# Optimization experiments

Hardware: AMD Instinct MI355X
Metric: run time of the kernel (lower is better)

The kernel has to match this reference:

```python
import jax, jax.numpy as jnp
import numpy as np

B, T, C = 4, 2048, 1024
H, D = 16, 64  # num_heads, head_dim
SCALE = D ** -0.5


def setup_inputs() -> dict:
    key = jax.random.key(0)
    ks = jax.random.split(key, 6)
    s = 0.02
    return {
        "hidden_states": jax.random.normal(ks[0], (B, T, C), dtype=jnp.float32),
        "wq": jax.random.normal(ks[1], (C, C), dtype=jnp.float32) * s,
        "wk": jax.random.normal(ks[2], (C, C), dtype=jnp.float32) * s,
        "wv": jax.random.normal(ks[3], (C, C), dtype=jnp.float32) * s,
        "wo": jax.random.normal(ks[4], (C, C), dtype=jnp.float32) * s,
        "bo": jnp.zeros((C,), dtype=jnp.float32),
    }


def reference(hidden_states, wq, wk, wv, wo, bo):
    b, t, c = hidden_states.shape
    # torch nn.Linear: y = x @ W^T
    q = hidden_states @ wq.T
    k = hidden_states @ wk.T
    v = hidden_states @ wv.T
    # (b, t, c) -> (b, h, t, d)
    q = q.reshape(b, t, H, D).transpose(0, 2, 1, 3)
    k = k.reshape(b, t, H, D).transpose(0, 2, 1, 3)
    v = v.reshape(b, t, H, D).transpose(0, 2, 1, 3)
    scores = jnp.einsum("bhqd,bhkd->bhqk", q, k) * SCALE
    attn = jax.nn.softmax(scores, axis=-1)
    out = jnp.einsum("bhqk,bhkd->bhqd", attn, v)
    out = out.transpose(0, 2, 1, 3).reshape(b, t, c)
    return out @ wo.T + bo
```

## Files before the change

### kernel.cpp

```cpp
#include <hip/hip_runtime.h>
#include <hip/hip_bf16.h>
#include <stdint.h>
#include <math.h>

#define Bb 4
#define Tt 2048
#define Cc 1024
#define Hh 16
#define Dd 64
#define Mm (Bb * Tt)
#define KVB 64
#define NT (Tt / KVB)

typedef __attribute__((ext_vector_type(8))) short bf8;
typedef __attribute__((ext_vector_type(4))) float f32x4;
typedef __attribute__((ext_vector_type(16))) float f32x16;
typedef __attribute__((ext_vector_type(8))) float f32x8v;
typedef __attribute__((ext_vector_type(2))) float f32x2v;
typedef __attribute__((ext_vector_type(8))) unsigned short u16x8;

#define QSCALE 0.1803368801111244f
#define M_FIX 4.0f

__device__ __forceinline__ unsigned short f2bf(float f) {
  __hip_bfloat16 h = __float2bfloat16(f);
  return *reinterpret_cast<unsigned short*>(&h);
}
__device__ __forceinline__ float bf2f(unsigned short s) {
  union { unsigned u; float f; } v; v.u = ((unsigned)s) << 16;
  return v.f;
}
__device__ __forceinline__ float fexp2(float x) {
#if __has_builtin(__builtin_amdgcn_exp2f)
  return __builtin_amdgcn_exp2f(x);
#else
  return exp2f(x);
#endif
}
__device__ __forceinline__ unsigned cvtpk(float lo, float hi) {
  unsigned r;
  asm volatile("v_cvt_pk_bf16_f32 %0, %1, %2" : "=v"(r) : "v"(lo), "v"(hi));
  return r;
}
__device__ __forceinline__ void gl_lds16(const void* g, void* l) {
  __builtin_amdgcn_global_load_lds(
      (const __attribute__((address_space(1))) void*)g,
      (__attribute__((address_space(3))) void*)l, 16, 0, 0);
}

__global__ __launch_bounds__(256) void cast_all(
    const float* __restrict__ hs, const float* __restrict__ wq,
    const float* __restrict__ wk, const float* __restrict__ wv,
    const float* __restrict__ wo, unsigned short* __restrict__ Xb,
    unsigned short* __restrict__ Wbase) {
  long long g = (long long)(blockIdx.x * 256 + threadIdx.x) * 8;
  const float* src;
  unsigned short* dst;
  long long off;
  const long long HS = 8LL * 1024 * 1024;
  if (g < HS) {
    src = hs; dst = Xb; off = g;
  } else {
    long long r = g - HS;
    int wsel = (int)(r >> 20);
    off = r & ((1LL << 20) - 1);
    src = (wsel == 0) ? wq : (wsel == 1) ? wk : (wsel == 2) ? wv : wo;
    dst = Wbase + ((long long)wsel << 20);
  }
  const float4* p = (const float4*)(src + off);
  float4 a = p[0], b = p[1];
  u16x8 o;
  o[0] = f2bf(a.x); o[1] = f2bf(a.y); o[2] = f2bf(a.z); o[3] = f2bf(a.w);
  o[4] = f2bf(b.x); o[5] = f2bf(b.y); o[6] = f2bf(b.z); o[7] = f2bf(b.w);
  *(u16x8*)(dst + off) = o;
}

template <int MODE>
__global__ __launch_bounds__(256, 2)
void gemm_bt(const unsigned short* __restrict__ A,
             const unsigned short* __restrict__ Bw,
             void* __restrict__ Cout,
             const float* __restrict__ bias,
             int M, int N, int K) {
  __shared__ unsigned short As[128 * 32];
  __shared__ unsigned short Bs[128 * 32];
  const int tid = threadIdx.x;
  const int lane = tid & 63;
  const int w = tid >> 6;
  const int wr = w >> 1, wc = w & 1;
  const int row0 = blockIdx.y * 128;
  const int col0 = blockIdx.x * 128;
  const int lr = lane & 15;
  const int lk = (lane >> 4) * 8;

  f32x4 acc[4][4] = {};

  const int sr = tid >> 2;
  const int sc = (tid & 3) * 8;

  for (int k0 = 0; k0 < K; k0 += 32) {
    gl_lds16(A  + (size_t)(row0 + sr) * K + k0 + sc,      &As[sr * 32 + sc]);
    gl_lds16(A  + (size_t)(row0 + 64 + sr) * K + k0 + sc, &As[(64 + sr) * 32 + sc]);
    gl_lds16(Bw + (size_t)(col0 + sr) * K + k0 + sc,      &Bs[sr * 32 + sc]);
    gl_lds16(Bw + (size_t)(col0 + 64 + sr) * K + k0 + sc, &Bs[(64 + sr) * 32 + sc]);
    __syncthreads();

    bf8 a[4], b[4];
#pragma unroll
    for (int mi = 0; mi < 4; ++mi)
      a[mi] = *(const bf8*)&As[(wr * 64 + mi * 16 + lr) * 32 + lk];
#pragma unroll
    for (int ni = 0; ni < 4; ++ni)
      b[ni] = *(const bf8*)&Bs[(wc * 64 + ni * 16 + lr) * 32 + lk];
#pragma unroll
    for (int mi = 0; mi < 4; ++mi)
#pragma unroll
      for (int ni = 0; ni < 4; ++ni)
        acc[mi][ni] = __builtin_amdgcn_mfma_f32_16x16x32_bf16(
            a[mi], b[ni], acc[mi][ni], 0, 0, 0);
    __syncthreads();
  }

#pragma unroll
  for (int mi = 0; mi < 4; ++mi) {
#pragma unroll
    for (int ni = 0; ni < 4; ++ni) {
      const int col = col0 + wc * 64 + ni * 16 + lr;
      const int rowb = row0 + wr * 64 + mi * 16 + (lane >> 4) * 4;
      if (MODE == 1) {
#pragma unroll
        for (int r = 0; r < 4; ++r)
          ((float*)Cout)[(size_t)(rowb + r) * N + col] = acc[mi][ni][r] + bias[col];
      } else {
        unsigned short* outb = (unsigned short*)Cout;
        if (col < 2048) {
          unsigned short* dst = outb + (col < 1024 ? 0 : 8 * 1024 * 1024);
          const int c = col & 1023;
#pragma unroll
          for (int r = 0; r < 4; ++r)
            dst[(size_t)(rowb + r) * 1024 + c] = f2bf(acc[mi][ni][r]);
        } else {
          const int c = col - 2048;
          const int bidx = rowb >> 11, t0 = rowb & 2047;
          const int hh = c >> 6, dd = c & 63;
          uint2 pk;
          pk.x = (unsigned)f2bf(acc[mi][ni][0]) | ((unsigned)f2bf(acc[mi][ni][1]) << 16);
          pk.y = (unsigned)f2bf(acc[mi][ni][2]) | ((unsigned)f2bf(acc[mi][ni][3]) << 16);
          size_t addr = (((size_t)(bidx * Hh + hh)) * Dd + dd) * (size_t)Tt + t0;
          *(uint2*)(outb + 16 * 1024 * 1024 + addr) = pk;
        }
      }
    }
  }
}

__global__ __launch_bounds__(512, 2)
void flash_attn(const unsigned short* __restrict__ Q,
                const unsigned short* __restrict__ Km,
                const unsigned short* __restrict__ Vt,
                unsigned short* __restrict__ O) {
  __shared__ unsigned short smem[3 * 8192];

  const int tid = threadIdx.x;
  const int lane = tid & 63;
  const int w = tid >> 6;
  const int bh = blockIdx.x;
  const int qt = blockIdx.y;
  const int b = bh >> 4, h = bh & 15;
  const size_t base = (size_t)b * Tt * Cc + (size_t)h * Dd;
  const size_t vtbase = (size_t)bh * Dd * Tt;
  const int r31 = lane & 31, hi = lane >> 5;
  const int qrow = qt * 256 + w * 32 + r31;
  const int sw = r31 & 7;

  int coh[4];
#pragma unroll
  for (int ks = 0; ks < 4; ++ks) coh[ks] = ((2 * ks + hi) ^ sw) * 8;

  bf8 qb[4];
#pragma unroll
  for (int ks = 0; ks < 4; ++ks) {
    bf8 t = *(const bf8*)(Q + base + (size_t)qrow * Cc + ks * 16 + hi * 8);
#pragma unroll
    for (int i = 0; i < 8; ++i)
      qb[ks][i] = (short)f2bf(bf2f((unsigned short)t[i]) * QSCALE);
  }

  float l_r = 0.f;
  f32x16 o_acc[2];
#pragma unroll
  for (int dt = 0; dt < 2; ++dt) o_acc[dt] = (f32x16)0.0f;

  const int strow = tid >> 3;
  const int stch = tid & 7;
  const unsigned short* ksrc = Km + base + (size_t)strow * Cc + ((stch ^ (strow & 7)) * 8);
  const unsigned short* vsrc = Vt + vtbase + (size_t)strow * Tt + ((stch ^ (strow & 7)) * 8);

  gl_lds16(ksrc,                   &smem[0 * 8192 + tid * 8]);
  gl_lds16(vsrc,                   &smem[0 * 8192 + 4096 + tid * 8]);
  gl_lds16(ksrc + (size_t)KVB * Cc, &smem[1 * 8192 + tid * 8]);
  gl_lds16(vsrc + KVB,             &smem[1 * 8192 + 4096 + tid * 8]);
  asm volatile("s_waitcnt vmcnt(2)" ::: "memory");
  __builtin_amdgcn_sched_barrier(0);
  __builtin_amdgcn_s_barrier();
  __builtin_amdgcn_sched_barrier(0);

  int cur = 0;
  for (int t = 0; t < NT; ++t) {
    if (t + 2 < NT) {
      int nb = cur + 2; if (nb >= 3) nb -= 3;
      const int kb = (t + 2) * KVB;
      gl_lds16(ksrc + (size_t)kb * Cc, &smem[nb * 8192 + tid * 8]);
      gl_lds16(vsrc + kb,              &smem[nb * 8192 + 4096 + tid * 8]);
    }

    const unsigned short* ksl = &smem[cur * 8192];
    const unsigned short* vsl = &smem[cur * 8192 + 4096];

    f32x16 s0 = (f32x16)0.0f, s1 = (f32x16)0.0f;
    __builtin_amdgcn_s_setprio(1);
#pragma unroll
    for (int ks = 0; ks < 4; ++ks) {
      bf8 kf = *(const bf8*)&ksl[r31 * 64 + coh[ks]];
      s0 = __builtin_amdgcn_mfma_f32_32x32x16_bf16(kf, qb[ks], s0, 0, 0, 0);
    }
#pragma unroll
    for (int ks = 0; ks < 4; ++ks) {
      bf8 kf = *(const bf8*)&ksl[(32 + r31) * 64 + coh[ks]];
      s1 = __builtin_amdgcn_mfma_f32_32x32x16_bf16(kf, qb[ks], s1, 0, 0, 0);
    }
    __builtin_amdgcn_s_setprio(0);

    s0 = s0 - M_FIX;
    s1 = s1 - M_FIX;
#pragma unroll
    for (int j = 0; j < 16; ++j) { s0[j] = fexp2(s0[j]); s1[j] = fexp2(s1[j]); }
    {
      f32x16 t16 = s0 + s1;
      f32x8v t8v = __builtin_shufflevector(t16, t16, 0, 1, 2, 3, 4, 5, 6, 7) +
                   __builtin_shufflevector(t16, t16, 8, 9, 10, 11, 12, 13, 14, 15);
      f32x4 t4v = __builtin_shufflevector(t8v, t8v, 0, 1, 2, 3) +
                  __builtin_shufflevector(t8v, t8v, 4, 5, 6, 7);
      f32x2v t2v = __builtin_shufflevector(t4v, t4v, 0, 1) +
                   __builtin_shufflevector(t4v, t4v, 2, 3);
      float ps = t2v[0] + t2v[1];
      ps += __shfl_xor(ps, 32);
      l_r += ps;
    }

    unsigned U[8][2];
#pragma unroll
    for (int k = 0; k < 4; ++k) {
      U[k][0] = cvtpk(s0[4 * k],     s0[4 * k + 1]);
      U[k][1] = cvtpk(s0[4 * k + 2], s0[4 * k + 3]);
      U[4 + k][0] = cvtpk(s1[4 * k],     s1[4 * k + 1]);
      U[4 + k][1] = cvtpk(s1[4 * k + 2], s1[4 * k + 3]);
    }
    bf8 pb[4];
#pragma unroll
    for (int ks = 0; ks < 4; ++ks) {
      unsigned a0 = U[2 * ks][0], b0 = U[2 * ks + 1][0];
      asm volatile("v_permlane32_swap_b32 %0, %1" : "+v"(a0), "+v"(b0));
      unsigned a1 = U[2 * ks][1], b1 = U[2 * ks + 1][1];
      asm volatile("v_permlane32_swap_b32 %0, %1" : "+v"(a1), "+v"(b1));
      union { unsigned u[4]; bf8 v; } pk_;
      pk_.u[0] = a0; pk_.u[1] = a1; pk_.u[2] = b0; pk_.u[3] = b1;
      pb[ks] = pk_.v;
    }

    __builtin_amdgcn_s_setprio(1);
#pragma unroll
    for (int dt = 0; dt < 2; ++dt) {
      f32x16 z = o_acc[dt];
#pragma unroll
      for (int ks = 0; ks < 4; ++ks) {
        bf8 vf = *(const bf8*)&vsl[(dt * 32 + r31) * 64 + coh[ks]];
        z = __builtin_amdgcn_mfma_f32_32x32x16_bf16(vf, pb[ks], z, 0, 0, 0);
      }
      o_acc[dt] = z;
    }
    __builtin_amdgcn_s_setprio(0);

    if (t + 2 < NT) {
      asm volatile("s_waitcnt vmcnt(2)" ::: "memory");
    } else {
      asm volatile("s_waitcnt vmcnt(0)" ::: "memory");
    }
    __builtin_amdgcn_sched_barrier(0);
    __builtin_amdgcn_s_barrier();
    __builtin_amdgcn_sched_barrier(0);
    cur = cur + 1; if (cur >= 3) cur -= 3;
  }

  const float linv = 1.0f / l_r;
#pragma unroll
  for (int dt = 0; dt < 2; ++dt) {
    f32x16 on = o_acc[dt] * linv;
#pragma unroll
    for (int g = 0; g < 4; ++g) {
      uint2 pk;
      pk.x = (unsigned)f2bf(on[4 * g]) | ((unsigned)f2bf(on[4 * g + 1]) << 16);
      pk.y = (unsigned)f2bf(on[4 * g + 2]) | ((unsigned)f2bf(on[4 * g + 3]) << 16);
      *(uint2*)(O + base + (size_t)qrow * Cc + dt * 32 + g * 8 + hi * 4) = pk;
    }
  }
}

extern "C" void kernel_launch(void* const* d_in, const int* in_sizes, int n_in,
                              void* d_out, int out_size, void* d_ws, size_t ws_size,
                              hipStream_t stream) {
  (void)in_sizes; (void)n_in; (void)out_size; (void)ws_size;
  const float* hs = (const float*)d_in[0];
  const float* wq = (const float*)d_in[1];
  const float* wk = (const float*)d_in[2];
  const float* wv = (const float*)d_in[3];
  const float* wo = (const float*)d_in[4];
  const float* bo = (const float*)d_in[5];

  char* ws = (char*)d_ws;
  const size_t MB = 1u << 20;
  unsigned short* Xb  = (unsigned short*)(ws + 0);
  unsigned short* Wqb = (unsigned short*)(ws + 16 * MB);
  unsigned short* Wob = (unsigned short*)(ws + 22 * MB);
  unsigned short* Qb  = (unsigned short*)(ws + 24 * MB);
  unsigned short* Kb  = (unsigned short*)(ws + 40 * MB);
  unsigned short* Vtb = (unsigned short*)(ws + 56 * MB);
  unsigned short* Ob  = Xb;

  cast_all<<<6144, 256, 0, stream>>>(hs, wq, wk, wv, wo, Xb, Wqb);

  gemm_bt<3><<<dim3(24, 64), 256, 0, stream>>>(Xb, Wqb, Qb, nullptr, Mm, 3072, Cc);

  flash_attn<<<dim3(Bb * Hh, Tt / 256), 512, 0, stream>>>(Qb, Kb, Vtb, Ob);

  gemm_bt<1><<<dim3(8, 64), 256, 0, stream>>>(Ob, Wob, (float*)d_out, bo, Mm, Cc, Cc);
}
```

Before: 193.1 us.

## Triple-buffer LDS staging in bf16 GEMM with async prefetch two tiles ahead

Replaces the single-buffered LDS tile load in the projection GEMM with a three-stage ring buffer. Global-to-LDS loads for tile t+2 are issued before computing tile t, and explicit vmcnt waits plus one barrier per iteration replace the two __syncthreads. MFMA sections are also wrapped in s_setprio to favor math issue. This aims to hide global memory latency, at the cost of more LDS per block (48KB), which may limit occupancy at two blocks per CU.

```diff
diff --git a/kernel.cpp b/kernel.cpp
--- a/kernel.cpp
+++ b/kernel.cpp
@@ -82,8 +82,7 @@
              void* __restrict__ Cout,
              const float* __restrict__ bias,
              int M, int N, int K) {
-  __shared__ unsigned short As[128 * 32];
-  __shared__ unsigned short Bs[128 * 32];
+  __shared__ unsigned short smem[3 * 8192];
   const int tid = threadIdx.x;
   const int lane = tid & 63;
   const int w = tid >> 6;
@@ -97,29 +96,67 @@
 
   const int sr = tid >> 2;
   const int sc = (tid & 3) * 8;
-
-  for (int k0 = 0; k0 < K; k0 += 32) {
-    gl_lds16(A  + (size_t)(row0 + sr) * K + k0 + sc,      &As[sr * 32 + sc]);
-    gl_lds16(A  + (size_t)(row0 + 64 + sr) * K + k0 + sc, &As[(64 + sr) * 32 + sc]);
-    gl_lds16(Bw + (size_t)(col0 + sr) * K + k0 + sc,      &Bs[sr * 32 + sc]);
-    gl_lds16(Bw + (size_t)(col0 + 64 + sr) * K + k0 + sc, &Bs[(64 + sr) * 32 + sc]);
-    __syncthreads();
+  const int NK = K >> 5;
+
+  const unsigned short* a0p = A  + (size_t)(row0 + sr) * K + sc;
+  const unsigned short* a1p = A  + (size_t)(row0 + 64 + sr) * K + sc;
+  const unsigned short* b0p = Bw + (size_t)(col0 + sr) * K + sc;
+  const unsigned short* b1p = Bw + (size_t)(col0 + 64 + sr) * K + sc;
+
+#define STAGE(kt, buf)                                                   \
+  {                                                                      \
+    unsigned short* As_ = &smem[(buf) * 8192];                           \
+    unsigned short* Bs_ = &smem[(buf) * 8192 + 4096];                    \
+    const int k0_ = (kt) * 32;                                           \
+    gl_lds16(a0p + k0_, &As_[sr * 32 + sc]);                             \
+    gl_lds16(a1p + k0_, &As_[(64 + sr) * 32 + sc]);                      \
+    gl_lds16(b0p + k0_, &Bs_[sr * 32 + sc]);                             \
+    gl_lds16(b1p + k0_, &Bs_[(64 + sr) * 32 + sc]);                      \
+  }
+
+  STAGE(0, 0)
+  STAGE(1, 1)
+  asm volatile("s_waitcnt vmcnt(4)" ::: "memory");
+  __builtin_amdgcn_sched_barrier(0);
+  __builtin_amdgcn_s_barrier();
+  __builtin_amdgcn_sched_barrier(0);
+
+  int cur = 0;
+  for (int t = 0; t < NK; ++t) {
+    if (t + 2 < NK) {
+      int nb = cur + 2; if (nb >= 3) nb -= 3;
+      STAGE(t + 2, nb)
+    }
+    const unsigned short* As_ = &smem[cur * 8192];
+    const unsigned short* Bs_ = &smem[cur * 8192 + 4096];
 
     bf8 a[4], b[4];
 #pragma unroll
     for (int mi = 0; mi < 4; ++mi)
-      a[mi] = *(const bf8*)&As[(wr * 64 + mi * 16 + lr) * 32 + lk];
+      a[mi] = *(const bf8*)&As_[(wr * 64 + mi * 16 + lr) * 32 + lk];
 #pragma unroll
     for (int ni = 0; ni < 4; ++ni)
-      b[ni] = *(const bf8*)&Bs[(wc * 64 + ni * 16 + lr) * 32 + lk];
+      b[ni] = *(const bf8*)&Bs_[(wc * 64 + ni * 16 + lr) * 32 + lk];
+    __builtin_amdgcn_s_setprio(1);
 #pragma unroll
     for (int mi = 0; mi < 4; ++mi)
 #pragma unroll
       for (int ni = 0; ni < 4; ++ni)
         acc[mi][ni] = __builtin_amdgcn_mfma_f32_16x16x32_bf16(
             a[mi], b[ni], acc[mi][ni], 0, 0, 0);
-    __syncthreads();
-  }
+    __builtin_amdgcn_s_setprio(0);
+
+    if (t + 2 < NK) {
+      asm volatile("s_waitcnt vmcnt(4)" ::: "memory");
+    } else {
+      asm volatile("s_waitcnt vmcnt(0)" ::: "memory");
+    }
+    __builtin_amdgcn_sched_barrier(0);
+    __builtin_amdgcn_s_barrier();
+    __builtin_amdgcn_sched_barrier(0);
+    cur = cur + 1; if (cur >= 3) cur -= 3;
+  }
+#undef STAGE
 
 #pragma unroll
   for (int mi = 0; mi < 4; ++mi) {
```

Result: faster. 188.8 us (-2.2%).
